# Optimization experiments

Measured on AMD Instinct MI355X. Metric: run time of the kernel, lower is better.

## Reference

```python
import jax, jax.numpy as jnp
import numpy as np

N_EMBD = 1024
N_HEAD = 16
HEAD_SIZE = N_EMBD // N_HEAD  # 64


def rotate_half(x):
    x1, x2 = x[..., : x.shape[-1] // 2], x[..., x.shape[-1] // 2 :]
    return jnp.concatenate([-x2, x1], axis=-1)


def rope_cos_sin(T, head_size, dtype):
    inv_freq = 1.0 / (10000.0 ** (jnp.arange(0, head_size, 2, dtype=jnp.float32) / head_size))
    t = jnp.arange(T, dtype=jnp.float32)
    freqs = jnp.outer(t, inv_freq)  # (T, D/2)
    emb = jnp.concatenate([freqs, freqs], axis=-1)  # (T, D)
    return jnp.cos(emb).astype(dtype), jnp.sin(emb).astype(dtype)


def setup_inputs() -> dict:
    key = jax.random.key(0)
    k1, k2, k3, k4 = jax.random.split(key, 4)
    B, T, C = 4, 4096, N_EMBD
    scale = 1.0 / np.sqrt(C)
    return {
        "x": jax.random.normal(k1, (B, T, C), dtype=jnp.float32),
        "sigma0": jnp.zeros((B, N_HEAD, HEAD_SIZE, HEAD_SIZE), dtype=jnp.float32),
        "w_qkv": jax.random.normal(k2, (3 * C, C), dtype=jnp.float32) * scale,
        "w_proj": jax.random.normal(k3, (C, C), dtype=jnp.float32) * scale,
        "eta": jnp.ones((1,), dtype=jnp.float32) * 0.1,
    }


def reference(x, sigma0, w_qkv, w_proj, eta):
    B, T, C = x.shape
    H, D = N_HEAD, HEAD_SIZE
    qkv = x @ w_qkv.T  # (B,T,3C)
    q, k, v = jnp.split(qkv, 3, axis=-1)
    # (B,T,C) -> (B,H,T,D)
    q = q.reshape(B, T, H, D).transpose(0, 2, 1, 3)
    k = k.reshape(B, T, H, D).transpose(0, 2, 1, 3)
    v = v.reshape(B, T, H, D).transpose(0, 2, 1, 3)
    cos, sin = rope_cos_sin(T, D, x.dtype)  # (T,D) broadcast over (B,H,T,D)
    q = q * cos + rotate_half(q) * sin
    k = k * cos + rotate_half(k) * sin
    q = jax.nn.relu(q)
    k = jax.nn.relu(k)
    # sequential Hebbian fast-weight scan over time
    q_t = q.transpose(2, 0, 1, 3)  # (T,B,H,D)
    k_t = k.transpose(2, 0, 1, 3)
    v_t = v.transpose(2, 0, 1, 3)
    eta_s = eta[0]

    def step(sigma, qkv_step):
        qt, kt, vt = qkv_step  # each (B,H,D)
        out_t = jnp.einsum("bhd,bhde->bhe", qt, sigma)  # read BEFORE update
        sigma = sigma + eta_s * jnp.einsum("bhd,bhe->bhde", kt, vt)
        return sigma, out_t

    sigma_final, outs = jax.lax.scan(step, sigma0, (q_t, k_t, v_t))
    # outs: (T,B,H,D) -> (B,T,C)
    out = outs.transpose(1, 0, 2, 3).reshape(B, T, C)
    out = out @ w_proj.T
    return out, sigma_final
```

## Files before the change

### kernel.cpp

```cpp
#include <hip/hip_runtime.h>
#include <hip/hip_bf16.h>
#include <cstdint>
#include <cstddef>

#define B_   4
#define T_   4096
#define C_   1024
#define H_   16
#define NC_  64
#define M_   (B_*T_)
#define N3_  (3*C_)
#define NT2  32

typedef __attribute__((ext_vector_type(4))) float  f32x4;
typedef __attribute__((ext_vector_type(8))) __bf16 bf16x8;
typedef __attribute__((ext_vector_type(4))) __bf16 bf16x4;
typedef __attribute__((ext_vector_type(8))) unsigned short u16x8;

__device__ __forceinline__ void glds16(void* lds, const void* g) {
  __builtin_amdgcn_global_load_lds((const __attribute__((address_space(1))) void*)g,
                                   (__attribute__((address_space(3))) void*)lds,
                                   16, 0, 0);
}
#define MFMA_BF16 __builtin_amdgcn_mfma_f32_16x16x32_bf16

__global__ __launch_bounds__(256) void cvt_f32_bf16(const float* __restrict__ in,
                                                    __bf16* __restrict__ out, int n4) {
  int i = blockIdx.x * 256 + threadIdx.x;
  if (i >= n4) return;
  float4 v = reinterpret_cast<const float4*>(in)[i];
  bf16x4 o;
  o[0] = (__bf16)v.x; o[1] = (__bf16)v.y; o[2] = (__bf16)v.z; o[3] = (__bf16)v.w;
  reinterpret_cast<bf16x4*>(out)[i] = o;
}

__global__ __launch_bounds__(256) void rope_tab(float2* __restrict__ tab) {
  int gid = blockIdx.x * 256 + threadIdx.x;
  int t = gid >> 5, dp = gid & 31;
  float invf = exp2f(-(float)dp * (13.287712379549449f / 32.0f));
  float ang = (float)t * invf;
  float s, c;
  sincosf(ang, &s, &c);
  tab[gid] = make_float2(c, s);
}

template<int FUSE>
__global__ __launch_bounds__(512) void gemm_pipe256(const __bf16* __restrict__ A,
                                                    const __bf16* __restrict__ Bt,
                                                    void* __restrict__ Cout,
                                                    const float2* __restrict__ tab,
                                                    int N) {
  __shared__ __bf16 sA[4][256 * 32];
  __shared__ __bf16 sB[4][256 * 32];
  const int tid  = threadIdx.x;
  const int lane = tid & 63;
  const int wave = tid >> 6;
  const int wm = wave >> 2, wn = wave & 3;
  const int bm = blockIdx.y, bn = blockIdx.x;
  const int fr = lane & 15, kq = lane >> 4;
  const int K = C_;

  const int r_loc = tid >> 2;
  const int sslot = (tid & 3) ^ (r_loc & 3);
  const __bf16* Ag = A  + (size_t)(bm * 256 + r_loc) * K + sslot * 8;
  const __bf16* Bg = Bt + (size_t)(bn * 256 + r_loc) * K + sslot * 8;

  f32x4 acc[8][4];
#pragma unroll
  for (int i = 0; i < 8; i++)
#pragma unroll
    for (int j = 0; j < 4; j++) acc[i][j] = (f32x4)0.0f;

#pragma unroll
  for (int t = 0; t < 3; ++t) {
    glds16((char*)sA[t] +    0 + tid * 16, Ag + (size_t)0 * 128 * K + t * 32);
    glds16((char*)sA[t] + 8192 + tid * 16, Ag + (size_t)1 * 128 * K + t * 32);
    glds16((char*)sB[t] +    0 + tid * 16, Bg + (size_t)0 * 128 * K + t * 32);
    glds16((char*)sB[t] + 8192 + tid * 16, Bg + (size_t)1 * 128 * K + t * 32);
  }
  asm volatile("s_waitcnt vmcnt(8)" ::: "memory");
  __builtin_amdgcn_sched_barrier(0);
  __builtin_amdgcn_s_barrier();

  const int swz = (kq ^ (fr & 3)) * 16;
  bf16x8 af[8], bf4[4];
  for (int t = 0; t < NT2; ++t) {
    const int buf  = t & 3;
    const int nbuf = (t + 3) & 3;
    const __bf16* Ab = (const __bf16*)sA[buf];
    const __bf16* Bb = (const __bf16*)sB[buf];

    if (t + 3 < NT2) {
      const int kb3 = (t + 3) * 32;
      glds16((char*)sA[nbuf] +    0 + tid * 16, Ag + (size_t)0 * 128 * K + kb3);
      glds16((char*)sA[nbuf] + 8192 + tid * 16, Ag + (size_t)1 * 128 * K + kb3);
      glds16((char*)sB[nbuf] +    0 + tid * 16, Bg + (size_t)0 * 128 * K + kb3);
      glds16((char*)sB[nbuf] + 8192 + tid * 16, Bg + (size_t)1 * 128 * K + kb3);
    }

#pragma unroll
    for (int i = 0; i < 8; ++i)
      af[i] = *(const bf16x8*)((const char*)Ab + (wm * 128 + i * 16 + fr) * 64 + swz);
#pragma unroll
    for (int j = 0; j < 4; ++j)
      bf4[j] = *(const bf16x8*)((const char*)Bb + (wn * 64 + j * 16 + fr) * 64 + swz);

    __builtin_amdgcn_s_setprio(1);
#pragma unroll
    for (int i = 0; i < 8; ++i)
#pragma unroll
      for (int j = 0; j < 4; ++j)
        acc[i][j] = MFMA_BF16(af[i], bf4[j], acc[i][j], 0, 0, 0);
    __builtin_amdgcn_s_setprio(0);

    if (t < NT2 - 1) {
      if (t < NT2 - 3)       asm volatile("s_waitcnt vmcnt(8)" ::: "memory");
      else if (t == NT2 - 3) asm volatile("s_waitcnt vmcnt(4)" ::: "memory");
      else                   asm volatile("s_waitcnt vmcnt(0)" ::: "memory");
      __builtin_amdgcn_sched_barrier(0);
      __builtin_amdgcn_s_barrier();
    }
  }

  const int rg4 = kq * 4;
  const int cb = bn * 256 + wn * 64;
  if (FUSE == 1 && bn < 8) {
#pragma unroll
    for (int i = 0; i < 8; ++i)
#pragma unroll
      for (int r = 0; r < 4; ++r) {
        size_t row = (size_t)bm * 256 + wm * 128 + i * 16 + rg4 + r;
        int tt = (int)(row & (T_ - 1));
#pragma unroll
        for (int j = 0; j < 2; ++j) {
          int dp = j * 16 + fr;
          float2 cs = tab[tt * 32 + dp];
          float x1 = acc[i][j][r], x2 = acc[i][j + 2][r];
          float o1 = fmaxf(x1 * cs.x - x2 * cs.y, 0.0f);
          float o2 = fmaxf(x2 * cs.x + x1 * cs.y, 0.0f);
          ((__bf16*)Cout)[row * N + cb + j * 16 + fr]      = (__bf16)o1;
          ((__bf16*)Cout)[row * N + cb + j * 16 + fr + 32] = (__bf16)o2;
        }
      }
  } else {
#pragma unroll
    for (int i = 0; i < 8; ++i)
#pragma unroll
      for (int j = 0; j < 4; ++j) {
        size_t row = (size_t)bm * 256 + wm * 128 + i * 16 + rg4;
        size_t col = (size_t)cb + j * 16 + fr;
#pragma unroll
        for (int r = 0; r < 4; ++r) {
          if (FUSE == 2) ((float*)Cout)[(row + r) * N + col]  = acc[i][j][r];
          else           ((__bf16*)Cout)[(row + r) * N + col] = (__bf16)acc[i][j][r];
        }
      }
  }
}

#define LDW 72
__global__ __launch_bounds__(256) void chunk_kv(const __bf16* __restrict__ qkv,
                                                __bf16* __restrict__ G) {
  __shared__ __bf16 Kt[64 * LDW];
  __shared__ __bf16 Vt[64 * LDW];
  const int bid = blockIdx.x;
  const int c = bid & (NC_ - 1);
  const int bh = bid >> 6;
  const int h = bh & (H_ - 1);
  const int b = bh >> 4;
  const int tid = threadIdx.x;
  const size_t row0 = (size_t)b * T_ + c * 64;
  const int kcol = C_ + h * 64;
  const int vcol = 2 * C_ + h * 64;
#pragma unroll
  for (int it = 0; it < 2; ++it) {
    int task = tid + it * 256;
    int t = task >> 3;
    int d0 = (task & 7) * 8;
    const size_t rb = (row0 + t) * N3_;
    u16x8 kv = *(const u16x8*)(qkv + rb + kcol + d0);
    u16x8 vv = *(const u16x8*)(qkv + rb + vcol + d0);
#pragma unroll
    for (int j = 0; j < 8; j++) {
      ((unsigned short*)Kt)[(d0 + j) * LDW + t] = kv[j];
      ((unsigned short*)Vt)[(d0 + j) * LDW + t] = vv[j];
    }
  }
  __syncthreads();
  const int lane = tid & 63, wave = tid >> 6;
  const int gr = (wave >> 1) * 32, gc = (wave & 1) * 32;
  const int fr = lane & 15, kb = (lane >> 4) * 8;
  f32x4 acc[2][2];
#pragma unroll
  for (int i = 0; i < 2; i++)
#pragma unroll
    for (int j = 0; j < 2; j++) acc[i][j] = (f32x4)0.0f;
#pragma unroll
  for (int kk = 0; kk < 2; ++kk) {
    bf16x8 af[2], bfr[2];
#pragma unroll
    for (int i = 0; i < 2; i++)
      af[i] = *(const bf16x8*)(Kt + (gr + i * 16 + fr) * LDW + kk * 32 + kb);
#pragma unroll
    for (int j = 0; j < 2; j++)
      bfr[j] = *(const bf16x8*)(Vt + (gc + j * 16 + fr) * LDW + kk * 32 + kb);
#pragma unroll
    for (int i = 0; i < 2; i++)
#pragma unroll
      for (int j = 0; j < 2; j++)
        acc[i][j] = MFMA_BF16(af[i], bfr[j], acc[i][j], 0, 0, 0);
  }
  const int rg = (lane >> 4) * 4;
  __bf16* Gb = G + (size_t)bid * 4096;
#pragma unroll
  for (int i = 0; i < 2; i++)
#pragma unroll
    for (int j = 0; j < 2; j++)
#pragma unroll
      for (int r = 0; r < 4; r++)
        Gb[(gr + i * 16 + rg + r) * 64 + gc + j * 16 + fr] = (__bf16)acc[i][j][r];
}

__global__ __launch_bounds__(256) void prefix_scan(const __bf16* __restrict__ G,
                                                   const float* __restrict__ sigma0,
                                                   __bf16* __restrict__ S,
                                                   float* __restrict__ sigma_out,
                                                   const float* __restrict__ eta) {
  const int blk = blockIdx.x;
  const int bh = blk >> 2;
  const int dq = blk & 3;
  const int tid = threadIdx.x;
  const int d = dq * 16 + (tid >> 4);
  const int e0 = (tid & 15) * 4;
  const float eta_s = eta[0];
  const size_t base_de = (size_t)d * 64 + e0;
  float acc[4], s0[4];
#pragma unroll
  for (int j = 0; j < 4; j++) {
    acc[j] = 0.0f;
    s0[j] = sigma0[(size_t)bh * 4096 + base_de + j];
  }
  for (int c = 0; c < NC_; ++c) {
    const size_t off = ((size_t)bh * NC_ + c) * 4096 + base_de;
    bf16x4 sv;
#pragma unroll
    for (int j = 0; j < 4; j++) sv[j] = (__bf16)(s0[j] + eta_s * acc[j]);
    *(bf16x4*)(S + off) = sv;
    bf16x4 g = *(const bf16x4*)(G + off);
#pragma unroll
    for (int j = 0; j < 4; j++) acc[j] += (float)g[j];
  }
  float4 v;
  v.x = s0[0] + eta_s * acc[0];
  v.y = s0[1] + eta_s * acc[1];
  v.z = s0[2] + eta_s * acc[2];
  v.w = s0[3] + eta_s * acc[3];
  *reinterpret_cast<float4*>(sigma_out + (size_t)bh * 4096 + base_de) = v;
}

__global__ __launch_bounds__(256) void chunk_out(const __bf16* __restrict__ qkv,
                                                 const __bf16* __restrict__ S,
                                                 __bf16* __restrict__ outp,
                                                 const float* __restrict__ eta) {
  __shared__ __bf16 Qs[64 * LDW];
  __shared__ __bf16 Ks[64 * LDW];
  __shared__ __bf16 Vt[64 * LDW];
  __shared__ __bf16 St[64 * LDW];
  __shared__ __bf16 Ps[64 * LDW];
  const int bid = blockIdx.x;
  const int c = bid & 63, bh = bid >> 6, h = bh & 15, b = bh >> 4;
  const int tid = threadIdx.x;
  const size_t row0 = (size_t)b * T_ + c * 64;
  const float eta_s = eta[0];
#pragma unroll
  for (int it = 0; it < 2; ++it) {
    int task = tid + it * 256;
    int t = task >> 3, d0 = (task & 7) * 8;
    const size_t rb = (row0 + t) * N3_;
    *(u16x8*)(Qs + t * LDW + d0) = *(const u16x8*)(qkv + rb + h * 64 + d0);
    *(u16x8*)(Ks + t * LDW + d0) = *(const u16x8*)(qkv + rb + C_ + h * 64 + d0);
    u16x8 vv = *(const u16x8*)(qkv + rb + 2 * C_ + h * 64 + d0);
    u16x8 sv = *(const u16x8*)(S + (size_t)bid * 4096 + t * 64 + d0);
#pragma unroll
    for (int j = 0; j < 8; j++) {
      ((unsigned short*)Vt)[(d0 + j) * LDW + t] = vv[j];
      ((unsigned short*)St)[(d0 + j) * LDW + t] = sv[j];
    }
  }
  __syncthreads();
  const int lane = tid & 63, wave = tid >> 6;
  const int qr = (wave >> 1) * 32, qc = (wave & 1) * 32;
  const int fr = lane & 15, kb = (lane >> 4) * 8, rg = (lane >> 4) * 4;
  {
    f32x4 pacc[2][2];
#pragma unroll
    for (int i = 0; i < 2; i++)
#pragma unroll
      for (int j = 0; j < 2; j++) pacc[i][j] = (f32x4)0.0f;
#pragma unroll
    for (int kk = 0; kk < 2; ++kk) {
      bf16x8 af[2], bfr[2];
#pragma unroll
      for (int i = 0; i < 2; i++)
        af[i] = *(const bf16x8*)(Qs + (qr + i * 16 + fr) * LDW + kk * 32 + kb);
#pragma unroll
      for (int j = 0; j < 2; j++)
        bfr[j] = *(const bf16x8*)(Ks + (qc + j * 16 + fr) * LDW + kk * 32 + kb);
#pragma unroll
      for (int i = 0; i < 2; i++)
#pragma unroll
        for (int j = 0; j < 2; j++)
          pacc[i][j] = MFMA_BF16(af[i], bfr[j], pacc[i][j], 0, 0, 0);
    }
#pragma unroll
    for (int i = 0; i < 2; i++)
#pragma unroll
      for (int j = 0; j < 2; j++)
#pragma unroll
        for (int r = 0; r < 4; r++) {
          int trow = qr + i * 16 + rg + r;
          int scol = qc + j * 16 + fr;
          float v = (scol < trow) ? eta_s * pacc[i][j][r] : 0.0f;
          Ps[trow * LDW + scol] = (__bf16)v;
        }
  }
  __syncthreads();
  {
    f32x4 oacc[2][2];
#pragma unroll
    for (int i = 0; i < 2; i++)
#pragma unroll
      for (int j = 0; j < 2; j++) oacc[i][j] = (f32x4)0.0f;
#pragma unroll
    for (int kk = 0; kk < 2; ++kk) {
      bf16x8 pa[2], vb[2], qa[2], sb[2];
#pragma unroll
      for (int i = 0; i < 2; i++) {
        pa[i] = *(const bf16x8*)(Ps + (qr + i * 16 + fr) * LDW + kk * 32 + kb);
        qa[i] = *(const bf16x8*)(Qs + (qr + i * 16 + fr) * LDW + kk * 32 + kb);
      }
#pragma unroll
      for (int j = 0; j < 2; j++) {
        vb[j] = *(const bf16x8*)(Vt + (qc + j * 16 + fr) * LDW + kk * 32 + kb);
        sb[j] = *(const bf16x8*)(St + (qc + j * 16 + fr) * LDW + kk * 32 + kb);
      }
#pragma unroll
      for (int i = 0; i < 2; i++)
#pragma unroll
        for (int j = 0; j < 2; j++) {
          oacc[i][j] = MFMA_BF16(pa[i], vb[j], oacc[i][j], 0, 0, 0);
          oacc[i][j] = MFMA_BF16(qa[i], sb[j], oacc[i][j], 0, 0, 0);
        }
    }
#pragma unroll
    for (int i = 0; i < 2; i++)
#pragma unroll
      for (int j = 0; j < 2; j++)
#pragma unroll
        for (int r = 0; r < 4; r++) {
          size_t row = row0 + qr + i * 16 + rg + r;
          int col = h * 64 + qc + j * 16 + fr;
          outp[row * C_ + col] = (__bf16)oacc[i][j][r];
        }
  }
}

extern "C" void kernel_launch(void* const* d_in, const int* in_sizes, int n_in,
                              void* d_out, int out_size, void* d_ws, size_t ws_size,
                              hipStream_t stream) {
  const float* x      = (const float*)d_in[0];
  const float* sigma0 = (const float*)d_in[1];
  const float* w_qkv  = (const float*)d_in[2];
  const float* w_proj = (const float*)d_in[3];
  const float* eta    = (const float*)d_in[4];
  float* out       = (float*)d_out;
  float* sigma_out = out + (size_t)M_ * C_;

  char* ws = (char*)d_ws;
  __bf16* xbf     = (__bf16*)(ws);
  __bf16* wqkvbf  = (__bf16*)(ws + 33554432);
  __bf16* wprojbf = (__bf16*)(ws + 39845888);
  __bf16* qkvbf   = (__bf16*)(ws + 41943040);
  __bf16* Gws     = (__bf16*)(ws + 142606336);
  __bf16* Sws     = (__bf16*)(ws + 176160768);
  float2* tab     = (float2*)(ws + 176160768);

  rope_tab<<<512, 256, 0, stream>>>(tab);
  cvt_f32_bf16<<<16384, 256, 0, stream>>>(x, xbf, 4194304);
  cvt_f32_bf16<<<3072, 256, 0, stream>>>(w_qkv, wqkvbf, 786432);
  cvt_f32_bf16<<<1024, 256, 0, stream>>>(w_proj, wprojbf, 262144);
  gemm_pipe256<1><<<dim3(12, 64), 512, 0, stream>>>(xbf, wqkvbf, (void*)qkvbf, tab, N3_);
  chunk_kv<<<4096, 256, 0, stream>>>(qkvbf, Gws);
  prefix_scan<<<256, 256, 0, stream>>>(Gws, sigma0, Sws, sigma_out, eta);
  chunk_out<<<4096, 256, 0, stream>>>(qkvbf, Sws, xbf, eta);
  gemm_pipe256<2><<<dim3(4, 64), 512, 0, stream>>>(xbf, wprojbf, (void*)out, nullptr, C_);
}
```

Baseline: 310.4 us.

## Switch GEMM to double-buffered 64-wide K tiles with 8-slot XOR swizzle

```diff
diff --git a/kernel.cpp b/kernel.cpp
--- a/kernel.cpp
+++ b/kernel.cpp
@@ -10,7 +10,7 @@
 #define NC_  64
 #define M_   (B_*T_)
 #define N3_  (3*C_)
-#define NT2  32
+#define NTK  16
 
 typedef __attribute__((ext_vector_type(4))) float  f32x4;
 typedef __attribute__((ext_vector_type(8))) __bf16 bf16x8;
@@ -45,23 +45,24 @@
 }
 
 template<int FUSE>
-__global__ __launch_bounds__(512) void gemm_pipe256(const __bf16* __restrict__ A,
-                                                    const __bf16* __restrict__ Bt,
-                                                    void* __restrict__ Cout,
-                                                    const float2* __restrict__ tab,
-                                                    int N) {
-  __shared__ __bf16 sA[4][256 * 32];
-  __shared__ __bf16 sB[4][256 * 32];
+__global__ __launch_bounds__(512) void gemm_dbuf(const __bf16* __restrict__ A,
+                                                 const __bf16* __restrict__ Bt,
+                                                 void* __restrict__ Cout,
+                                                 const float2* __restrict__ tab,
+                                                 int N) {
+  __shared__ __bf16 sA[2][256 * 64];
+  __shared__ __bf16 sB[2][256 * 64];
   const int tid  = threadIdx.x;
   const int lane = tid & 63;
   const int wave = tid >> 6;
   const int wm = wave >> 2, wn = wave & 3;
   const int bm = blockIdx.y, bn = blockIdx.x;
   const int fr = lane & 15, kq = lane >> 4;
+  const int fr7 = fr & 7;
   const int K = C_;
 
-  const int r_loc = tid >> 2;
-  const int sslot = (tid & 3) ^ (r_loc & 3);
+  const int r_loc = tid >> 3;
+  const int sslot = (tid & 7) ^ (r_loc & 7);
   const __bf16* Ag = A  + (size_t)(bm * 256 + r_loc) * K + sslot * 8;
   const __bf16* Bg = Bt + (size_t)(bn * 256 + r_loc) * K + sslot * 8;
 
@@ -72,51 +73,57 @@
     for (int j = 0; j < 4; j++) acc[i][j] = (f32x4)0.0f;
 
 #pragma unroll
-  for (int t = 0; t < 3; ++t) {
-    glds16((char*)sA[t] +    0 + tid * 16, Ag + (size_t)0 * 128 * K + t * 32);
-    glds16((char*)sA[t] + 8192 + tid * 16, Ag + (size_t)1 * 128 * K + t * 32);
-    glds16((char*)sB[t] +    0 + tid * 16, Bg + (size_t)0 * 128 * K + t * 32);
-    glds16((char*)sB[t] + 8192 + tid * 16, Bg + (size_t)1 * 128 * K + t * 32);
-  }
-  asm volatile("s_waitcnt vmcnt(8)" ::: "memory");
+  for (int q = 0; q < 4; ++q) {
+    glds16((char*)sA[0] + q * 8192 + tid * 16, Ag + (size_t)q * 64 * K);
+    glds16((char*)sB[0] + q * 8192 + tid * 16, Bg + (size_t)q * 64 * K);
+  }
+  asm volatile("s_waitcnt vmcnt(0)" ::: "memory");
   __builtin_amdgcn_sched_barrier(0);
   __builtin_amdgcn_s_barrier();
 
-  const int swz = (kq ^ (fr & 3)) * 16;
-  bf16x8 af[8], bf4[4];
-  for (int t = 0; t < NT2; ++t) {
-    const int buf  = t & 3;
-    const int nbuf = (t + 3) & 3;
+  bf16x8 af[4][2], bfr[4][2];
+  for (int t = 0; t < NTK; ++t) {
+    const int buf = t & 1, nb = buf ^ 1;
     const __bf16* Ab = (const __bf16*)sA[buf];
     const __bf16* Bb = (const __bf16*)sB[buf];
 
-    if (t + 3 < NT2) {
-      const int kb3 = (t + 3) * 32;
-      glds16((char*)sA[nbuf] +    0 + tid * 16, Ag + (size_t)0 * 128 * K + kb3);
-      glds16((char*)sA[nbuf] + 8192 + tid * 16, Ag + (size_t)1 * 128 * K + kb3);
-      glds16((char*)sB[nbuf] +    0 + tid * 16, Bg + (size_t)0 * 128 * K + kb3);
-      glds16((char*)sB[nbuf] + 8192 + tid * 16, Bg + (size_t)1 * 128 * K + kb3);
-    }
-
-#pragma unroll
-    for (int i = 0; i < 8; ++i)
-      af[i] = *(const bf16x8*)((const char*)Ab + (wm * 128 + i * 16 + fr) * 64 + swz);
+    if (t + 1 < NTK) {
+      const int kb = (t + 1) * 64;
+#pragma unroll
+      for (int q = 0; q < 4; ++q) {
+        glds16((char*)sA[nb] + q * 8192 + tid * 16, Ag + (size_t)q * 64 * K + kb);
+        glds16((char*)sB[nb] + q * 8192 + tid * 16, Bg + (size_t)q * 64 * K + kb);
+      }
+    }
+
 #pragma unroll
     for (int j = 0; j < 4; ++j)
-      bf4[j] = *(const bf16x8*)((const char*)Bb + (wn * 64 + j * 16 + fr) * 64 + swz);
-
-    __builtin_amdgcn_s_setprio(1);
-#pragma unroll
-    for (int i = 0; i < 8; ++i)
-#pragma unroll
-      for (int j = 0; j < 4; ++j)
-        acc[i][j] = MFMA_BF16(af[i], bf4[j], acc[i][j], 0, 0, 0);
-    __builtin_amdgcn_s_setprio(0);
-
-    if (t < NT2 - 1) {
-      if (t < NT2 - 3)       asm volatile("s_waitcnt vmcnt(8)" ::: "memory");
-      else if (t == NT2 - 3) asm volatile("s_waitcnt vmcnt(4)" ::: "memory");
-      else                   asm volatile("s_waitcnt vmcnt(0)" ::: "memory");
+#pragma unroll
+      for (int kk = 0; kk < 2; ++kk)
+        bfr[j][kk] = *(const bf16x8*)((const char*)Bb + (wn * 64 + j * 16 + fr) * 128 +
+                                      (((kk << 2) | kq) ^ fr7) * 16);
+#pragma unroll
+    for (int h = 0; h < 2; ++h) {
+#pragma unroll
+      for (int i = 0; i < 4; ++i)
+#pragma unroll
+        for (int kk = 0; kk < 2; ++kk)
+          af[i][kk] = *(const bf16x8*)((const char*)Ab +
+                        (wm * 128 + (h * 4 + i) * 16 + fr) * 128 +
+                        (((kk << 2) | kq) ^ fr7) * 16);
+      __builtin_amdgcn_s_setprio(1);
+#pragma unroll
+      for (int i = 0; i < 4; ++i)
+#pragma unroll
+        for (int j = 0; j < 4; ++j) {
+          acc[h * 4 + i][j] = MFMA_BF16(af[i][0], bfr[j][0], acc[h * 4 + i][j], 0, 0, 0);
+          acc[h * 4 + i][j] = MFMA_BF16(af[i][1], bfr[j][1], acc[h * 4 + i][j], 0, 0, 0);
+        }
+      __builtin_amdgcn_s_setprio(0);
+    }
+
+    if (t < NTK - 1) {
+      asm volatile("s_waitcnt vmcnt(0)" ::: "memory");
       __builtin_amdgcn_sched_barrier(0);
       __builtin_amdgcn_s_barrier();
     }
@@ -389,9 +396,9 @@
   cvt_f32_bf16<<<16384, 256, 0, stream>>>(x, xbf, 4194304);
   cvt_f32_bf16<<<3072, 256, 0, stream>>>(w_qkv, wqkvbf, 786432);
   cvt_f32_bf16<<<1024, 256, 0, stream>>>(w_proj, wprojbf, 262144);
-  gemm_pipe256<1><<<dim3(12, 64), 512, 0, stream>>>(xbf, wqkvbf, (void*)qkvbf, tab, N3_);
+  gemm_dbuf<1><<<dim3(12, 64), 512, 0, stream>>>(xbf, wqkvbf, (void*)qkvbf, tab, N3_);
   chunk_kv<<<4096, 256, 0, stream>>>(qkvbf, Gws);
   prefix_scan<<<256, 256, 0, stream>>>(Gws, sigma0, Sws, sigma_out, eta);
   chunk_out<<<4096, 256, 0, stream>>>(qkvbf, Sws, xbf, eta);
-  gemm_pipe256<2><<<dim3(4, 64), 512, 0, stream>>>(xbf, wprojbf, (void*)out, nullptr, C_);
-}
+  gemm_dbuf<2><<<dim3(4, 64), 512, 0, stream>>>(xbf, wprojbf, (void*)out, nullptr, C_);
+}
```

After: 267.7 us. -13.7%, faster.
